# Optimization experiments

Measured on AMD Instinct MI355X. Metric: run time of the kernel, lower is better.

Reference implementation:

```python
import jax, jax.numpy as jnp
import numpy as np

B, S, L, D, C_ENC, H = 8, 4096, 77, 1280, 2048, 20
DH = D // H          # 64
SCALE = DH ** -0.5


def setup_inputs() -> dict:
    key = jax.random.key(0)
    ks = jax.random.split(key, 8)
    return {
        "hidden_states": jax.random.normal(ks[0], (B, S, D), jnp.float32),
        "encoder_hidden_states": jax.random.normal(ks[1], (B, L, C_ENC), jnp.float32),
        "region_state": jax.random.uniform(ks[2], (B, S, L), jnp.float32),
        "Wq": jax.random.normal(ks[3], (D, D), jnp.float32) * 0.02,
        "Wk": jax.random.normal(ks[4], (C_ENC, D), jnp.float32) * 0.02,
        "Wv": jax.random.normal(ks[5], (C_ENC, D), jnp.float32) * 0.02,
        "Wo": jax.random.normal(ks[6], (D, D), jnp.float32) * 0.02,
        "bo": jnp.zeros((D,), jnp.float32),
        "sigma": jnp.ones((1,), jnp.float32) * 14.6,
    }


def reference(hidden_states, encoder_hidden_states, region_state, Wq, Wk, Wv, Wo, bo, sigma):
    # QKV projections (dense GEMMs)
    q = (hidden_states @ Wq).reshape(B, S, H, DH)            # [B,S,H,dh]
    k = (encoder_hidden_states @ Wk).reshape(B, L, H, DH)    # [B,L,H,dh]
    v = (encoder_hidden_states @ Wv).reshape(B, L, H, DH)
    # scaled attention scores (baddbmm with beta=0 == plain scaled matmul)
    scores = jnp.einsum('bshd,blhd->bhsl', q, k) * SCALE      # [B,H,S,L]
    # region-prompt bias: weight_func(w, sigma, qk) = w * log(1 + 0.1*sigma) * qk.max()
    # repeat_interleave over heads == broadcast over the head axis
    bias = region_state * (jnp.log1p(sigma[0] * 0.1) * scores.max())  # [B,S,L]
    scores = scores + bias[:, None, :, :]
    probs = jax.nn.softmax(scores, axis=-1)
    out = jnp.einsum('bhsl,blhd->bshd', probs, v).reshape(B, S, D)
    # output projection (to_out[0]); to_out[1] is dropout (identity at eval)
    return out @ Wo + bo
```

## Files before the change

kernel.cpp:

```cpp
#include <hip/hip_runtime.h>
#include <hip/hip_bf16.h>
#include <math.h>

#define NB 8
#define NS 4096
#define NL 77
#define NLP 80
#define NLPV 96
#define ND 1280
#define NC 2048
#define NH 20
#define NDH 64
#define QK_SCALE 0.125f

typedef __attribute__((ext_vector_type(4))) float f32x4;
typedef __attribute__((ext_vector_type(8))) short bf16x8;

static __device__ __forceinline__ void gload_lds16(const void* g, void* l) {
  __builtin_amdgcn_global_load_lds(
      (const __attribute__((address_space(1))) void*)g,
      (__attribute__((address_space(3))) void*)l, 16, 0, 0);
}

#define BAR() do { asm volatile("" ::: "memory"); __builtin_amdgcn_s_barrier(); asm volatile("" ::: "memory"); } while (0)
#define LGKM0() asm volatile("s_waitcnt lgkmcnt(0)" ::: "memory")

__global__ void cvt_bf16_kern(const float* __restrict__ in,
                              __hip_bfloat16* __restrict__ out, long n)
{
  long i = ((long)blockIdx.x * blockDim.x + threadIdx.x) * 4;
  long stride = (long)gridDim.x * blockDim.x * 4;
  for (; i < n; i += stride) {
    float4 v = *reinterpret_cast<const float4*>(in + i);
    union { __hip_bfloat16 h[4]; ushort4 u; } r;
    r.h[0] = __float2bfloat16(v.x);
    r.h[1] = __float2bfloat16(v.y);
    r.h[2] = __float2bfloat16(v.z);
    r.h[3] = __float2bfloat16(v.w);
    *reinterpret_cast<ushort4*>(out + i) = r.u;
  }
}

__global__ void transpose_bf16_kern(const float* __restrict__ in,
                                    __hip_bfloat16* __restrict__ out,
                                    int rows, int cols)
{
  __shared__ float t[32][33];
  int c0 = blockIdx.x * 32, r0 = blockIdx.y * 32;
  int tx = threadIdx.x, ty = threadIdx.y;
  for (int i = ty; i < 32; i += 8) {
    int r = r0 + i, c = c0 + tx;
    t[i][tx] = (r < rows && c < cols) ? in[(long)r * cols + c] : 0.f;
  }
  __syncthreads();
  for (int i = ty; i < 32; i += 8) {
    int oc = c0 + i, orr = r0 + tx;
    if (oc < cols && orr < rows)
      out[(long)oc * rows + orr] = __float2bfloat16(t[tx][i]);
  }
}

__global__ __launch_bounds__(256)
void gemm_bt_kern(const __hip_bfloat16* __restrict__ A,
                  const __hip_bfloat16* __restrict__ Bt,
                  void* __restrict__ C, const float* __restrict__ bias,
                  int M, int N, int K, int mode)
{
  __shared__ __align__(16) __hip_bfloat16 As[128 * 32];
  __shared__ __align__(16) __hip_bfloat16 Bs[128 * 32];
  const int t = threadIdx.x;
  const int lane = t & 63;
  const int w = t >> 6;
  const int wm = w >> 1, wn = w & 1;
  const int lr = lane & 15, hi = lane >> 4, lk = hi * 8;
  const long m0 = (long)blockIdx.x * 128;
  const long n0 = (long)blockIdx.y * 128;

  f32x4 acc[4][4];
#pragma unroll
  for (int mi = 0; mi < 4; ++mi)
#pragma unroll
    for (int ni = 0; ni < 4; ++ni) acc[mi][ni] = {0.f, 0.f, 0.f, 0.f};

  for (int k0 = 0; k0 < K; k0 += 32) {
    __syncthreads();
#pragma unroll
    for (int rnd = 0; rnd < 2; ++rnd) {
      int idx = rnd * 256 + t;
      int row = idx >> 2, kpp = (idx & 3) * 8;
      long arow = m0 + row; if (arow >= M) arow = M - 1;
      gload_lds16(A + arow * K + k0 + kpp, (void*)(As + idx * 8));
      long brow = n0 + row;
      gload_lds16(Bt + brow * K + k0 + kpp, (void*)(Bs + idx * 8));
    }
    __syncthreads();

    bf16x8 af[4], bfr[4];
#pragma unroll
    for (int i = 0; i < 4; ++i) {
      af[i]  = *reinterpret_cast<const bf16x8*>(As + (wm * 64 + i * 16 + lr) * 32 + lk);
      bfr[i] = *reinterpret_cast<const bf16x8*>(Bs + (wn * 64 + i * 16 + lr) * 32 + lk);
    }
#pragma unroll
    for (int mi = 0; mi < 4; ++mi)
#pragma unroll
      for (int ni = 0; ni < 4; ++ni)
        acc[mi][ni] = __builtin_amdgcn_mfma_f32_16x16x32_bf16(af[mi], bfr[ni], acc[mi][ni], 0, 0, 0);
  }

#pragma unroll
  for (int mi = 0; mi < 4; ++mi) {
#pragma unroll
    for (int r = 0; r < 4; ++r) {
      long row = m0 + wm * 64 + mi * 16 + hi * 4 + r;
      if (row < M) {
#pragma unroll
        for (int ni = 0; ni < 4; ++ni) {
          long col = n0 + wn * 64 + ni * 16 + lr;
          if (mode == 0)
            ((__hip_bfloat16*)C)[row * N + col] = __float2bfloat16(acc[mi][ni][r]);
          else
            ((float*)C)[row * N + col] = acc[mi][ni][r] + bias[col];
        }
      }
    }
  }
}

__global__ __launch_bounds__(256, 2)
void gemm128_kern(const __hip_bfloat16* __restrict__ A,
                  const __hip_bfloat16* __restrict__ Bt,
                  void* __restrict__ C, const float* __restrict__ bias,
                  int M, int N, int K, int mode)
{
  __shared__ __align__(16) __hip_bfloat16 sm[32768];
  char* smc = (char*)sm;

  const int t = threadIdx.x, lane = t & 63, w = t >> 6;
  const int wm = w >> 1, wn = w & 1;
  const int lr = lane & 15, hi = lane >> 4;
  const int sw = lr & 7;

  int nwg = gridDim.x;
  int cpx = nwg >> 3;
  int swz = (blockIdx.x & 7) * cpx + (blockIdx.x >> 3);
  int nxt = N >> 7;
  int mt = swz / nxt, ntile = swz - mt * nxt;
  const long m0 = (long)mt * 128, n0 = (long)ntile * 128;

  const int srow  = t >> 3;
  const int skoff = ((t & 7) ^ (srow & 7)) * 8;
  const int sdst  = t * 16;

  f32x4 acc[4][4];
#pragma unroll
  for (int mi = 0; mi < 4; ++mi)
#pragma unroll
    for (int ni = 0; ni < 4; ++ni) acc[mi][ni] = {0.f, 0.f, 0.f, 0.f};

  auto stageA = [&](int b, int kt) {
#pragma unroll
    for (int c = 0; c < 4; ++c)
      gload_lds16(A + (m0 + c * 32 + srow) * (long)K + kt * 64 + skoff,
                  (void*)(smc + b * 16384 + c * 4096 + sdst));
  };
  auto stageB = [&](int b, int kt) {
#pragma unroll
    for (int c = 0; c < 4; ++c)
      gload_lds16(Bt + (n0 + c * 32 + srow) * (long)K + kt * 64 + skoff,
                  (void*)(smc + 32768 + b * 16384 + c * 4096 + sdst));
  };

  const int NT = K >> 6;
  stageA(0, 0); stageB(0, 0);
  stageA(1, 1); stageB(1, 1);
  asm volatile("s_waitcnt vmcnt(8)" ::: "memory");
  BAR();

  for (int t2 = 0; t2 < NT; ++t2) {
    const int b = t2 & 1;
    const char* pa = smc + b * 16384;
    const char* pb = smc + 32768 + b * 16384;
    const bool pf = (t2 + 2 < NT);

    bf16x8 af[4][2], bfr[4][2];
#pragma unroll
    for (int mi = 0; mi < 4; ++mi) {
      int row = wm * 64 + mi * 16 + lr;
#pragma unroll
      for (int kk = 0; kk < 2; ++kk)
        af[mi][kk] = *reinterpret_cast<const bf16x8*>(
            pa + row * 128 + ((((kk * 4 + hi) ^ sw)) << 4));
    }
#pragma unroll
    for (int ni = 0; ni < 4; ++ni) {
      int row = wn * 64 + ni * 16 + lr;
#pragma unroll
      for (int kk = 0; kk < 2; ++kk)
        bfr[ni][kk] = *reinterpret_cast<const bf16x8*>(
            pb + row * 128 + ((((kk * 4 + hi) ^ sw)) << 4));
    }
    __builtin_amdgcn_s_setprio(1);
#pragma unroll
    for (int mi = 0; mi < 4; ++mi)
#pragma unroll
      for (int ni = 0; ni < 4; ++ni) {
        acc[mi][ni] = __builtin_amdgcn_mfma_f32_16x16x32_bf16(af[mi][0], bfr[ni][0], acc[mi][ni], 0, 0, 0);
        acc[mi][ni] = __builtin_amdgcn_mfma_f32_16x16x32_bf16(af[mi][1], bfr[ni][1], acc[mi][ni], 0, 0, 0);
      }
    __builtin_amdgcn_s_setprio(0);

    LGKM0();
    BAR();
    if (pf) { stageA(b, t2 + 2); stageB(b, t2 + 2); }
    if (pf) { asm volatile("s_waitcnt vmcnt(8)" ::: "memory"); }
    else    { asm volatile("s_waitcnt vmcnt(0)" ::: "memory"); }
    BAR();
  }

  if (mode == 0) {
#pragma unroll
    for (int mi = 0; mi < 4; ++mi)
#pragma unroll
      for (int r = 0; r < 4; ++r) {
        long row = m0 + wm * 64 + mi * 16 + hi * 4 + r;
#pragma unroll
        for (int ni = 0; ni < 4; ++ni) {
          long col = n0 + wn * 64 + ni * 16 + lr;
          ((__hip_bfloat16*)C)[row * N + col] = __float2bfloat16(acc[mi][ni][r]);
        }
      }
  } else {
    float bv[4];
#pragma unroll
    for (int ni = 0; ni < 4; ++ni) bv[ni] = bias[n0 + wn * 64 + ni * 16 + lr];
#pragma unroll
    for (int mi = 0; mi < 4; ++mi)
#pragma unroll
      for (int r = 0; r < 4; ++r) {
        long row = m0 + wm * 64 + mi * 16 + hi * 4 + r;
#pragma unroll
        for (int ni = 0; ni < 4; ++ni) {
          long col = n0 + wn * 64 + ni * 16 + lr;
          ((float*)C)[row * N + col] = acc[mi][ni][r] + bv[ni];
        }
      }
  }
}

__global__ void repack_kv_kern(const __hip_bfloat16* __restrict__ kvc,
                               __hip_bfloat16* __restrict__ kp,
                               __hip_bfloat16* __restrict__ vt)
{
  int idx = blockIdx.x * 256 + threadIdx.x;
  const __hip_bfloat16 z = __float2bfloat16(0.f);
  if (idx < NB * NLP * ND) {
    int d = idx % ND;
    int l = (idx / ND) % NLP;
    int b = idx / (ND * NLP);
    kp[idx] = (l < NL) ? kvc[((long)(b * NL + l)) * 2560 + d] : z;
  }
  if (idx < NB * NH * NDH * NLPV) {
    int l  = idx % NLPV;
    int dh = (idx / NLPV) % NDH;
    int h  = (idx / (NLPV * NDH)) % NH;
    int b  = idx / (NLPV * NDH * NH);
    vt[idx] = (l < NL) ? kvc[((long)(b * NL + l)) * 2560 + ND + h * NDH + dh] : z;
  }
}

__global__ __launch_bounds__(256)
void qk_max_kern(const __hip_bfloat16* __restrict__ qb,
                 const __hip_bfloat16* __restrict__ kp,
                 float* __restrict__ bmax)
{
  int t = threadIdx.x, lane = t & 63, wi = t >> 6;
  int b = blockIdx.z, h = blockIdx.y;
  int lr = lane & 15, lk = (lane >> 4) * 8;

  bf16x8 bk[5][2];
#pragma unroll
  for (int lt = 0; lt < 5; ++lt) {
    const __hip_bfloat16* Kr = kp + ((long)(b * NLP + lt * 16 + lr)) * ND + h * NDH + lk;
    bk[lt][0] = *reinterpret_cast<const bf16x8*>(Kr);
    bk[lt][1] = *reinterpret_cast<const bf16x8*>(Kr + 32);
  }

  float m = -1e30f;
#pragma unroll
  for (int st = 0; st < 4; ++st) {
    int s0 = blockIdx.x * 256 + wi * 64 + st * 16;
    const __hip_bfloat16* Qp = qb + ((long)(b * NS + s0 + lr)) * ND + h * NDH + lk;
    bf16x8 aq0 = *reinterpret_cast<const bf16x8*>(Qp);
    bf16x8 aq1 = *reinterpret_cast<const bf16x8*>(Qp + 32);
#pragma unroll
    for (int lt = 0; lt < 5; ++lt) {
      f32x4 sc = {0.f, 0.f, 0.f, 0.f};
      sc = __builtin_amdgcn_mfma_f32_16x16x32_bf16(aq0, bk[lt][0], sc, 0, 0, 0);
      sc = __builtin_amdgcn_mfma_f32_16x16x32_bf16(aq1, bk[lt][1], sc, 0, 0, 0);
      bool valid = (lt < 4) || (lr < 13);
      if (valid) {
#pragma unroll
        for (int r = 0; r < 4; ++r) m = fmaxf(m, sc[r]);
      }
    }
  }
#pragma unroll
  for (int k = 32; k >= 1; k >>= 1) m = fmaxf(m, __shfl_xor(m, k));

  __shared__ float wmx[4];
  if (lane == 0) wmx[wi] = m;
  __syncthreads();
  if (t == 0) {
    float mm = fmaxf(fmaxf(wmx[0], wmx[1]), fmaxf(wmx[2], wmx[3]));
    long bid = ((long)blockIdx.z * gridDim.y + blockIdx.y) * gridDim.x + blockIdx.x;
    bmax[bid] = mm * QK_SCALE;
  }
}

__global__ void reduce_max_kern(const float* __restrict__ bm, int n,
                                const float* __restrict__ sigma,
                                float* __restrict__ cb)
{
  __shared__ float sm[256];
  float m = -1e30f;
  for (int i = threadIdx.x; i < n; i += 256) m = fmaxf(m, bm[i]);
  sm[threadIdx.x] = m;
  __syncthreads();
  for (int s = 128; s > 0; s >>= 1) {
    if (threadIdx.x < (unsigned)s) sm[threadIdx.x] = fmaxf(sm[threadIdx.x], sm[threadIdx.x + s]);
    __syncthreads();
  }
  if (threadIdx.x == 0) cb[0] = log1pf(sigma[0] * 0.1f) * sm[0];
}

__global__ __launch_bounds__(256)
void attn_kern(const __hip_bfloat16* __restrict__ qb,
               const __hip_bfloat16* __restrict__ kp,
               const __hip_bfloat16* __restrict__ vt,
               const float* __restrict__ rs,
               const float* __restrict__ cb,
               __hip_bfloat16* __restrict__ ao_out)
{
  __shared__ __align__(16) __hip_bfloat16 pl[4][16][NLPV];
  int t = threadIdx.x, lane = t & 63, wi = t >> 6;
  int b = blockIdx.z, h = blockIdx.y;
  int lr = lane & 15, hi = lane >> 4, lk = hi * 8;
  const float c = cb[0];

  bf16x8 bk[5][2];
#pragma unroll
  for (int lt = 0; lt < 5; ++lt) {
    const __hip_bfloat16* Kr = kp + ((long)(b * NLP + lt * 16 + lr)) * ND + h * NDH + lk;
    bk[lt][0] = *reinterpret_cast<const bf16x8*>(Kr);
    bk[lt][1] = *reinterpret_cast<const bf16x8*>(Kr + 32);
  }
#pragma unroll
  for (int r = 0; r < 4; ++r)
    pl[wi][hi * 4 + r][80 + lr] = __float2bfloat16(0.f);

  const __hip_bfloat16* Vb = vt + ((long)((b * NH + h) * NDH)) * NLPV;

#pragma unroll
  for (int st = 0; st < 4; ++st) {
    int s0 = blockIdx.x * 256 + wi * 64 + st * 16;
    const __hip_bfloat16* Qp = qb + ((long)(b * NS + s0 + lr)) * ND + h * NDH + lk;
    bf16x8 aq0 = *reinterpret_cast<const bf16x8*>(Qp);
    bf16x8 aq1 = *reinterpret_cast<const bf16x8*>(Qp + 32);

    f32x4 sc[5];
#pragma unroll
    for (int lt = 0; lt < 5; ++lt) {
      f32x4 z = {0.f, 0.f, 0.f, 0.f};
      z = __builtin_amdgcn_mfma_f32_16x16x32_bf16(aq0, bk[lt][0], z, 0, 0, 0);
      sc[lt] = __builtin_amdgcn_mfma_f32_16x16x32_bf16(aq1, bk[lt][1], z, 0, 0, 0);
    }

    float sv[5][4];
    float pm[4] = {-1e30f, -1e30f, -1e30f, -1e30f};
#pragma unroll
    for (int lt = 0; lt < 5; ++lt) {
      int l = lt * 16 + lr;
#pragma unroll
      for (int r = 0; r < 4; ++r) {
        if (l < NL) {
          int srow = s0 + hi * 4 + r;
          float v = sc[lt][r] * QK_SCALE + rs[((long)(b * NS + srow)) * NL + l] * c;
          sv[lt][r] = v;
          pm[r] = fmaxf(pm[r], v);
        } else {
          sv[lt][r] = -1e30f;
        }
      }
    }
#pragma unroll
    for (int r = 0; r < 4; ++r)
#pragma unroll
      for (int k = 8; k >= 1; k >>= 1) pm[r] = fmaxf(pm[r], __shfl_xor(pm[r], k));

    float p[5][4];
    float psum[4] = {0.f, 0.f, 0.f, 0.f};
#pragma unroll
    for (int lt = 0; lt < 5; ++lt) {
      int l = lt * 16 + lr;
#pragma unroll
      for (int r = 0; r < 4; ++r) {
        float e = (l < NL) ? __expf(sv[lt][r] - pm[r]) : 0.f;
        p[lt][r] = e;
        psum[r] += e;
      }
    }
#pragma unroll
    for (int r = 0; r < 4; ++r)
#pragma unroll
      for (int k = 8; k >= 1; k >>= 1) psum[r] += __shfl_xor(psum[r], k);
    float rinv[4];
#pragma unroll
    for (int r = 0; r < 4; ++r) rinv[r] = 1.f / psum[r];

    LGKM0();

#pragma unroll
    for (int lt = 0; lt < 5; ++lt)
#pragma unroll
      for (int r = 0; r < 4; ++r)
        pl[wi][hi * 4 + r][lt * 16 + lr] = __float2bfloat16(p[lt][r]);

    LGKM0();

    f32x4 ao[4];
#pragma unroll
    for (int nt = 0; nt < 4; ++nt) ao[nt] = {0.f, 0.f, 0.f, 0.f};
#pragma unroll
    for (int ks = 0; ks < 3; ++ks) {
      bf16x8 pa = *reinterpret_cast<const bf16x8*>(&pl[wi][lr][ks * 32 + lk]);
#pragma unroll
      for (int nt = 0; nt < 4; ++nt) {
        bf16x8 bv = *reinterpret_cast<const bf16x8*>(Vb + ((long)(nt * 16 + lr)) * NLPV + ks * 32 + lk);
        ao[nt] = __builtin_amdgcn_mfma_f32_16x16x32_bf16(pa, bv, ao[nt], 0, 0, 0);
      }
    }

#pragma unroll
    for (int nt = 0; nt < 4; ++nt)
#pragma unroll
      for (int r = 0; r < 4; ++r) {
        int srow = s0 + hi * 4 + r;
        ao_out[((long)(b * NS + srow)) * ND + h * NDH + nt * 16 + lr] =
            __float2bfloat16(ao[nt][r] * rinv[r]);
      }
  }
}

extern "C" void kernel_launch(void* const* d_in, const int* in_sizes, int n_in,
                              void* d_out, int out_size, void* d_ws, size_t ws_size,
                              hipStream_t stream)
{
  const float* hs    = (const float*)d_in[0];
  const float* ehs   = (const float*)d_in[1];
  const float* rs    = (const float*)d_in[2];
  const float* Wq    = (const float*)d_in[3];
  const float* Wk    = (const float*)d_in[4];
  const float* Wv    = (const float*)d_in[5];
  const float* Wo    = (const float*)d_in[6];
  const float* bo    = (const float*)d_in[7];
  const float* sigma = (const float*)d_in[8];
  float* out = (float*)d_out;

  char* ws = (char*)d_ws;
  size_t off = 0;
  auto alloc = [&](size_t bytes) {
    void* p = ws + off;
    off = (off + bytes + 255) & ~(size_t)255;
    return p;
  };
  __hip_bfloat16* hsb  = (__hip_bfloat16*)alloc((size_t)NB * NS * ND * 2);
  __hip_bfloat16* qb   = (__hip_bfloat16*)alloc((size_t)NB * NS * ND * 2);
  __hip_bfloat16* wqt  = (__hip_bfloat16*)alloc((size_t)ND * ND * 2);
  __hip_bfloat16* wkvt = (__hip_bfloat16*)alloc((size_t)2560 * NC * 2);
  __hip_bfloat16* wot  = (__hip_bfloat16*)alloc((size_t)ND * ND * 2);
  __hip_bfloat16* ehsb = (__hip_bfloat16*)alloc((size_t)NB * NL * NC * 2);
  __hip_bfloat16* kvc  = (__hip_bfloat16*)alloc((size_t)NB * NL * 2560 * 2);
  __hip_bfloat16* kp   = (__hip_bfloat16*)alloc((size_t)NB * NLP * ND * 2);
  __hip_bfloat16* vt   = (__hip_bfloat16*)alloc((size_t)NB * NH * NDH * NLPV * 2);
  float* bmax = (float*)alloc(10240 * 4);
  float* cb   = (float*)alloc(256);

  cvt_bf16_kern<<<2048, 256, 0, stream>>>(hs, hsb, (long)NB * NS * ND);
  cvt_bf16_kern<<<512, 256, 0, stream>>>(ehs, ehsb, (long)NB * NL * NC);

  transpose_bf16_kern<<<dim3(40, 40), dim3(32, 8), 0, stream>>>(Wq, wqt, ND, ND);
  transpose_bf16_kern<<<dim3(40, 64), dim3(32, 8), 0, stream>>>(Wk, wkvt, NC, ND);
  transpose_bf16_kern<<<dim3(40, 64), dim3(32, 8), 0, stream>>>(Wv, wkvt + (size_t)ND * NC, NC, ND);
  transpose_bf16_kern<<<dim3(40, 40), dim3(32, 8), 0, stream>>>(Wo, wot, ND, ND);

  gemm128_kern<<<2560, 256, 0, stream>>>(hsb, wqt, qb, nullptr, NB * NS, ND, ND, 0);

  gemm_bt_kern<<<dim3(5, 20), 256, 0, stream>>>(ehsb, wkvt, kvc, nullptr, NB * NL, 2560, NC, 0);

  repack_kv_kern<<<3840, 256, 0, stream>>>(kvc, kp, vt);

  qk_max_kern<<<dim3(16, NH, NB), 256, 0, stream>>>(qb, kp, bmax);
  reduce_max_kern<<<1, 256, 0, stream>>>(bmax, 16 * NH * NB, sigma, cb);

  attn_kern<<<dim3(16, NH, NB), 256, 0, stream>>>(qb, kp, vt, rs, cb, hsb);

  gemm128_kern<<<2560, 256, 0, stream>>>(hsb, wot, out, bo, NB * NS, ND, ND, 1);
}
```

Measured before the change: 502.5 us.

## Fuse fp32-to-bf16 conversion into Q GEMM and use single-buffered GEMM

Removes the standalone conversion kernel for hidden_states. The Q projection GEMM now loads fp32 tiles straight into LDS and converts them to bf16 while building MFMA fragments. The GEMM is also restructured: the double-buffered async prefetch pipeline is replaced by a single-buffered load, sync, compute loop, and launch bounds are raised to 4 blocks per CU so occupancy can hide latency. This saves a full read and write pass over the 8x4096x1280 activation, but A-tile traffic doubles in the GEMM and load/compute overlap inside a block is lost.

```diff
diff --git a/kernel.cpp b/kernel.cpp
--- a/kernel.cpp
+++ b/kernel.cpp
@@ -22,7 +22,6 @@
       (__attribute__((address_space(3))) void*)l, 16, 0, 0);
 }
 
-#define BAR() do { asm volatile("" ::: "memory"); __builtin_amdgcn_s_barrier(); asm volatile("" ::: "memory"); } while (0)
 #define LGKM0() asm volatile("s_waitcnt lgkmcnt(0)" ::: "memory")
 
 __global__ void cvt_bf16_kern(const float* __restrict__ in,
@@ -127,19 +126,19 @@
   }
 }
 
-__global__ __launch_bounds__(256, 2)
-void gemm128_kern(const __hip_bfloat16* __restrict__ A,
+template<bool AF32>
+__global__ __launch_bounds__(256, 4)
+void gemm_sb_kern(const void* __restrict__ Av,
                   const __hip_bfloat16* __restrict__ Bt,
                   void* __restrict__ C, const float* __restrict__ bias,
                   int M, int N, int K, int mode)
 {
-  __shared__ __align__(16) __hip_bfloat16 sm[32768];
-  char* smc = (char*)sm;
+  constexpr int ABYTES = AF32 ? 32768 : 16384;
+  __shared__ __align__(16) char smc[ABYTES + 16384];
 
   const int t = threadIdx.x, lane = t & 63, w = t >> 6;
   const int wm = w >> 1, wn = w & 1;
   const int lr = lane & 15, hi = lane >> 4;
-  const int sw = lr & 7;
 
   int nwg = gridDim.x;
   int cpx = nwg >> 3;
@@ -148,49 +147,70 @@
   int mt = swz / nxt, ntile = swz - mt * nxt;
   const long m0 = (long)mt * 128, n0 = (long)ntile * 128;
 
-  const int srow  = t >> 3;
-  const int skoff = ((t & 7) ^ (srow & 7)) * 8;
-  const int sdst  = t * 16;
-
   f32x4 acc[4][4];
 #pragma unroll
   for (int mi = 0; mi < 4; ++mi)
 #pragma unroll
     for (int ni = 0; ni < 4; ++ni) acc[mi][ni] = {0.f, 0.f, 0.f, 0.f};
 
-  auto stageA = [&](int b, int kt) {
-#pragma unroll
-    for (int c = 0; c < 4; ++c)
-      gload_lds16(A + (m0 + c * 32 + srow) * (long)K + kt * 64 + skoff,
-                  (void*)(smc + b * 16384 + c * 4096 + sdst));
-  };
-  auto stageB = [&](int b, int kt) {
-#pragma unroll
-    for (int c = 0; c < 4; ++c)
-      gload_lds16(Bt + (n0 + c * 32 + srow) * (long)K + kt * 64 + skoff,
-                  (void*)(smc + 32768 + b * 16384 + c * 4096 + sdst));
-  };
-
   const int NT = K >> 6;
-  stageA(0, 0); stageB(0, 0);
-  stageA(1, 1); stageB(1, 1);
-  asm volatile("s_waitcnt vmcnt(8)" ::: "memory");
-  BAR();
-
-  for (int t2 = 0; t2 < NT; ++t2) {
-    const int b = t2 & 1;
-    const char* pa = smc + b * 16384;
-    const char* pb = smc + 32768 + b * 16384;
-    const bool pf = (t2 + 2 < NT);
+  for (int kt = 0; kt < NT; ++kt) {
+    __syncthreads();
+    if constexpr (AF32) {
+      const float* A = (const float*)Av;
+      int row0 = t >> 4, slot = t & 15;
+      int eoff = (slot ^ row0) * 4;
+#pragma unroll
+      for (int c = 0; c < 8; ++c) {
+        int row = c * 16 + row0;
+        gload_lds16(A + (m0 + row) * (long)K + kt * 64 + eoff,
+                    (void*)(smc + c * 4096 + t * 16));
+      }
+    } else {
+      const __hip_bfloat16* A = (const __hip_bfloat16*)Av;
+      int row0 = t >> 3, slot = t & 7;
+      int eoff = (slot ^ (row0 & 7)) * 8;
+#pragma unroll
+      for (int c = 0; c < 4; ++c) {
+        int row = c * 32 + row0;
+        gload_lds16(A + (m0 + row) * (long)K + kt * 64 + eoff,
+                    (void*)(smc + c * 4096 + t * 16));
+      }
+    }
+    {
+      int row0 = t >> 3, slot = t & 7;
+      int eoff = (slot ^ (row0 & 7)) * 8;
+#pragma unroll
+      for (int c = 0; c < 4; ++c) {
+        int row = c * 32 + row0;
+        gload_lds16(Bt + (n0 + row) * (long)K + kt * 64 + eoff,
+                    (void*)(smc + ABYTES + c * 4096 + t * 16));
+      }
+    }
+    __syncthreads();
 
     bf16x8 af[4][2], bfr[4][2];
 #pragma unroll
     for (int mi = 0; mi < 4; ++mi) {
       int row = wm * 64 + mi * 16 + lr;
 #pragma unroll
-      for (int kk = 0; kk < 2; ++kk)
-        af[mi][kk] = *reinterpret_cast<const bf16x8*>(
-            pa + row * 128 + ((((kk * 4 + hi) ^ sw)) << 4));
+      for (int kk = 0; kk < 2; ++kk) {
+        if constexpr (AF32) {
+          int s0 = 8 * kk + 2 * hi;
+          f32x4 v0 = *reinterpret_cast<const f32x4*>(smc + row * 256 + (((s0)     ^ lr) << 4));
+          f32x4 v1 = *reinterpret_cast<const f32x4*>(smc + row * 256 + (((s0 + 1) ^ lr) << 4));
+          bf16x8 r;
+#pragma unroll
+          for (int e = 0; e < 4; ++e) {
+            r[e]     = (short)__bfloat16_as_ushort(__float2bfloat16(v0[e]));
+            r[e + 4] = (short)__bfloat16_as_ushort(__float2bfloat16(v1[e]));
+          }
+          af[mi][kk] = r;
+        } else {
+          af[mi][kk] = *reinterpret_cast<const bf16x8*>(
+              smc + row * 128 + (((kk * 4 + hi) ^ (lr & 7)) << 4));
+        }
+      }
     }
 #pragma unroll
     for (int ni = 0; ni < 4; ++ni) {
@@ -198,9 +218,8 @@
 #pragma unroll
       for (int kk = 0; kk < 2; ++kk)
         bfr[ni][kk] = *reinterpret_cast<const bf16x8*>(
-            pb + row * 128 + ((((kk * 4 + hi) ^ sw)) << 4));
-    }
-    __builtin_amdgcn_s_setprio(1);
+            smc + ABYTES + row * 128 + (((kk * 4 + hi) ^ (lr & 7)) << 4));
+    }
 #pragma unroll
     for (int mi = 0; mi < 4; ++mi)
 #pragma unroll
@@ -208,14 +227,6 @@
         acc[mi][ni] = __builtin_amdgcn_mfma_f32_16x16x32_bf16(af[mi][0], bfr[ni][0], acc[mi][ni], 0, 0, 0);
         acc[mi][ni] = __builtin_amdgcn_mfma_f32_16x16x32_bf16(af[mi][1], bfr[ni][1], acc[mi][ni], 0, 0, 0);
       }
-    __builtin_amdgcn_s_setprio(0);
-
-    LGKM0();
-    BAR();
-    if (pf) { stageA(b, t2 + 2); stageB(b, t2 + 2); }
-    if (pf) { asm volatile("s_waitcnt vmcnt(8)" ::: "memory"); }
-    else    { asm volatile("s_waitcnt vmcnt(0)" ::: "memory"); }
-    BAR();
   }
 
   if (mode == 0) {
@@ -474,7 +485,7 @@
     off = (off + bytes + 255) & ~(size_t)255;
     return p;
   };
-  __hip_bfloat16* hsb  = (__hip_bfloat16*)alloc((size_t)NB * NS * ND * 2);
+  __hip_bfloat16* aob  = (__hip_bfloat16*)alloc((size_t)NB * NS * ND * 2);
   __hip_bfloat16* qb   = (__hip_bfloat16*)alloc((size_t)NB * NS * ND * 2);
   __hip_bfloat16* wqt  = (__hip_bfloat16*)alloc((size_t)ND * ND * 2);
   __hip_bfloat16* wkvt = (__hip_bfloat16*)alloc((size_t)2560 * NC * 2);
@@ -486,7 +497,6 @@
   float* bmax = (float*)alloc(10240 * 4);
   float* cb   = (float*)alloc(256);
 
-  cvt_bf16_kern<<<2048, 256, 0, stream>>>(hs, hsb, (long)NB * NS * ND);
   cvt_bf16_kern<<<512, 256, 0, stream>>>(ehs, ehsb, (long)NB * NL * NC);
 
   transpose_bf16_kern<<<dim3(40, 40), dim3(32, 8), 0, stream>>>(Wq, wqt, ND, ND);
@@ -494,7 +504,7 @@
   transpose_bf16_kern<<<dim3(40, 64), dim3(32, 8), 0, stream>>>(Wv, wkvt + (size_t)ND * NC, NC, ND);
   transpose_bf16_kern<<<dim3(40, 40), dim3(32, 8), 0, stream>>>(Wo, wot, ND, ND);
 
-  gemm128_kern<<<2560, 256, 0, stream>>>(hsb, wqt, qb, nullptr, NB * NS, ND, ND, 0);
+  gemm_sb_kern<true><<<2560, 256, 0, stream>>>(hs, wqt, qb, nullptr, NB * NS, ND, ND, 0);
 
   gemm_bt_kern<<<dim3(5, 20), 256, 0, stream>>>(ehsb, wkvt, kvc, nullptr, NB * NL, 2560, NC, 0);
 
@@ -503,7 +513,7 @@
   qk_max_kern<<<dim3(16, NH, NB), 256, 0, stream>>>(qb, kp, bmax);
   reduce_max_kern<<<1, 256, 0, stream>>>(bmax, 16 * NH * NB, sigma, cb);
 
-  attn_kern<<<dim3(16, NH, NB), 256, 0, stream>>>(qb, kp, vt, rs, cb, hsb);
-
-  gemm128_kern<<<2560, 256, 0, stream>>>(hsb, wot, out, bo, NB * NS, ND, ND, 1);
-}
+  attn_kern<<<dim3(16, NH, NB), 256, 0, stream>>>(qb, kp, vt, rs, cb, aob);
+
+  gemm_sb_kern<false><<<2560, 256, 0, stream>>>(aob, wot, out, bo, NB * NS, ND, ND, 1);
+}
```

New measurement: 529.0 us. +5.3%, slower.

## Fuse QK max reduction into Q projection GEMM epilogue and reorder barrier

Applied to the files above, without the earlier changes.

The Q projection GEMM now runs after the K/V repack and, in a templated mode, writes its bf16 output tile into LDS and computes the per-tile max of QK^T scores against K directly in its epilogue. This removes the separate qk_max kernel, which re-read all of Q from global memory. The main loop also moves the LDS wait, barrier and next-tile prefetch to before the MFMA block, so global loads overlap with the math. The costs are a longer epilogue, extra K loads per block, and more registers in the GEMM.

```diff
diff --git a/kernel.cpp b/kernel.cpp
--- a/kernel.cpp
+++ b/kernel.cpp
@@ -127,11 +127,14 @@
   }
 }
 
+template<int MODE>
 __global__ __launch_bounds__(256, 2)
 void gemm128_kern(const __hip_bfloat16* __restrict__ A,
                   const __hip_bfloat16* __restrict__ Bt,
                   void* __restrict__ C, const float* __restrict__ bias,
-                  int M, int N, int K, int mode)
+                  const __hip_bfloat16* __restrict__ kp,
+                  float* __restrict__ bmax,
+                  int M, int N, int K)
 {
   __shared__ __align__(16) __hip_bfloat16 sm[32768];
   char* smc = (char*)sm;
@@ -200,6 +203,10 @@
         bfr[ni][kk] = *reinterpret_cast<const bf16x8*>(
             pb + row * 128 + ((((kk * 4 + hi) ^ sw)) << 4));
     }
+    LGKM0();
+    BAR();
+    if (pf) { stageA(b, t2 + 2); stageB(b, t2 + 2); }
+
     __builtin_amdgcn_s_setprio(1);
 #pragma unroll
     for (int mi = 0; mi < 4; ++mi)
@@ -210,27 +217,12 @@
       }
     __builtin_amdgcn_s_setprio(0);
 
-    LGKM0();
-    BAR();
-    if (pf) { stageA(b, t2 + 2); stageB(b, t2 + 2); }
     if (pf) { asm volatile("s_waitcnt vmcnt(8)" ::: "memory"); }
     else    { asm volatile("s_waitcnt vmcnt(0)" ::: "memory"); }
     BAR();
   }
 
-  if (mode == 0) {
-#pragma unroll
-    for (int mi = 0; mi < 4; ++mi)
-#pragma unroll
-      for (int r = 0; r < 4; ++r) {
-        long row = m0 + wm * 64 + mi * 16 + hi * 4 + r;
-#pragma unroll
-        for (int ni = 0; ni < 4; ++ni) {
-          long col = n0 + wn * 64 + ni * 16 + lr;
-          ((__hip_bfloat16*)C)[row * N + col] = __float2bfloat16(acc[mi][ni][r]);
-        }
-      }
-  } else {
+  if constexpr (MODE == 1) {
     float bv[4];
 #pragma unroll
     for (int ni = 0; ni < 4; ++ni) bv[ni] = bias[n0 + wn * 64 + ni * 16 + lr];
@@ -245,6 +237,70 @@
           ((float*)C)[row * N + col] = acc[mi][ni][r] + bv[ni];
         }
       }
+  } else {
+    __hip_bfloat16* qsl = (__hip_bfloat16*)smc;
+#pragma unroll
+    for (int mi = 0; mi < 4; ++mi)
+#pragma unroll
+      for (int r = 0; r < 4; ++r) {
+        int rowl = wm * 64 + mi * 16 + hi * 4 + r;
+        long row = m0 + rowl;
+#pragma unroll
+        for (int ni = 0; ni < 4; ++ni) {
+          int col = wn * 64 + ni * 16 + lr;
+          __hip_bfloat16 v = __float2bfloat16(acc[mi][ni][r]);
+          ((__hip_bfloat16*)C)[row * N + n0 + col] = v;
+          if constexpr (MODE == 2) {
+            int bw = (col >> 3) ^ (rowl & 7);
+            qsl[rowl * 128 + (bw << 3) + (col & 7)] = v;
+          }
+        }
+      }
+    if constexpr (MODE == 2) {
+      LGKM0();
+      BAR();
+      const int bb = (int)(m0 >> 12);
+      float mx = -1e30f;
+#pragma unroll
+      for (int hh = 0; hh < 2; ++hh) {
+        const int h = (int)(n0 >> 6) + hh;
+        bf16x8 bk0[5], bk1[5];
+#pragma unroll
+        for (int lt = 0; lt < 5; ++lt) {
+          const __hip_bfloat16* Kr = kp + ((long)(bb * NLP + lt * 16 + lr)) * ND + h * NDH + hi * 8;
+          bk0[lt] = *reinterpret_cast<const bf16x8*>(Kr);
+          bk1[lt] = *reinterpret_cast<const bf16x8*>(Kr + 32);
+        }
+#pragma unroll
+        for (int su = 0; su < 2; ++su) {
+          int qrow = (w * 2 + su) * 16 + lr;
+          int bi0 = (hh * 8 + hi)     ^ sw;
+          int bi1 = (hh * 8 + 4 + hi) ^ sw;
+          bf16x8 aq0 = *reinterpret_cast<const bf16x8*>(qsl + qrow * 128 + (bi0 << 3));
+          bf16x8 aq1 = *reinterpret_cast<const bf16x8*>(qsl + qrow * 128 + (bi1 << 3));
+#pragma unroll
+          for (int lt = 0; lt < 5; ++lt) {
+            f32x4 sc = {0.f, 0.f, 0.f, 0.f};
+            sc = __builtin_amdgcn_mfma_f32_16x16x32_bf16(aq0, bk0[lt], sc, 0, 0, 0);
+            sc = __builtin_amdgcn_mfma_f32_16x16x32_bf16(aq1, bk1[lt], sc, 0, 0, 0);
+            if ((lt < 4) || (lr < 13)) {
+#pragma unroll
+              for (int r = 0; r < 4; ++r) mx = fmaxf(mx, sc[r]);
+            }
+          }
+        }
+      }
+#pragma unroll
+      for (int k = 32; k >= 1; k >>= 1) mx = fmaxf(mx, __shfl_xor(mx, k));
+      float* wmx = (float*)(smc + 32768);
+      if (lane == 0) wmx[w] = mx;
+      LGKM0();
+      BAR();
+      if (t == 0) {
+        float mm = fmaxf(fmaxf(wmx[0], wmx[1]), fmaxf(wmx[2], wmx[3]));
+        bmax[blockIdx.x] = mm * QK_SCALE;
+      }
+    }
   }
 }
 
@@ -266,55 +322,6 @@
     int h  = (idx / (NLPV * NDH)) % NH;
     int b  = idx / (NLPV * NDH * NH);
     vt[idx] = (l < NL) ? kvc[((long)(b * NL + l)) * 2560 + ND + h * NDH + dh] : z;
-  }
-}
-
-__global__ __launch_bounds__(256)
-void qk_max_kern(const __hip_bfloat16* __restrict__ qb,
-                 const __hip_bfloat16* __restrict__ kp,
-                 float* __restrict__ bmax)
-{
-  int t = threadIdx.x, lane = t & 63, wi = t >> 6;
-  int b = blockIdx.z, h = blockIdx.y;
-  int lr = lane & 15, lk = (lane >> 4) * 8;
-
-  bf16x8 bk[5][2];
-#pragma unroll
-  for (int lt = 0; lt < 5; ++lt) {
-    const __hip_bfloat16* Kr = kp + ((long)(b * NLP + lt * 16 + lr)) * ND + h * NDH + lk;
-    bk[lt][0] = *reinterpret_cast<const bf16x8*>(Kr);
-    bk[lt][1] = *reinterpret_cast<const bf16x8*>(Kr + 32);
-  }
-
-  float m = -1e30f;
-#pragma unroll
-  for (int st = 0; st < 4; ++st) {
-    int s0 = blockIdx.x * 256 + wi * 64 + st * 16;
-    const __hip_bfloat16* Qp = qb + ((long)(b * NS + s0 + lr)) * ND + h * NDH + lk;
-    bf16x8 aq0 = *reinterpret_cast<const bf16x8*>(Qp);
-    bf16x8 aq1 = *reinterpret_cast<const bf16x8*>(Qp + 32);
-#pragma unroll
-    for (int lt = 0; lt < 5; ++lt) {
-      f32x4 sc = {0.f, 0.f, 0.f, 0.f};
-      sc = __builtin_amdgcn_mfma_f32_16x16x32_bf16(aq0, bk[lt][0], sc, 0, 0, 0);
-      sc = __builtin_amdgcn_mfma_f32_16x16x32_bf16(aq1, bk[lt][1], sc, 0, 0, 0);
-      bool valid = (lt < 4) || (lr < 13);
-      if (valid) {
-#pragma unroll
-        for (int r = 0; r < 4; ++r) m = fmaxf(m, sc[r]);
-      }
-    }
-  }
-#pragma unroll
-  for (int k = 32; k >= 1; k >>= 1) m = fmaxf(m, __shfl_xor(m, k));
-
-  __shared__ float wmx[4];
-  if (lane == 0) wmx[wi] = m;
-  __syncthreads();
-  if (t == 0) {
-    float mm = fmaxf(fmaxf(wmx[0], wmx[1]), fmaxf(wmx[2], wmx[3]));
-    long bid = ((long)blockIdx.z * gridDim.y + blockIdx.y) * gridDim.x + blockIdx.x;
-    bmax[bid] = mm * QK_SCALE;
   }
 }
 
@@ -494,16 +501,14 @@
   transpose_bf16_kern<<<dim3(40, 64), dim3(32, 8), 0, stream>>>(Wv, wkvt + (size_t)ND * NC, NC, ND);
   transpose_bf16_kern<<<dim3(40, 40), dim3(32, 8), 0, stream>>>(Wo, wot, ND, ND);
 
-  gemm128_kern<<<2560, 256, 0, stream>>>(hsb, wqt, qb, nullptr, NB * NS, ND, ND, 0);
-
   gemm_bt_kern<<<dim3(5, 20), 256, 0, stream>>>(ehsb, wkvt, kvc, nullptr, NB * NL, 2560, NC, 0);
-
   repack_kv_kern<<<3840, 256, 0, stream>>>(kvc, kp, vt);
 
-  qk_max_kern<<<dim3(16, NH, NB), 256, 0, stream>>>(qb, kp, bmax);
-  reduce_max_kern<<<1, 256, 0, stream>>>(bmax, 16 * NH * NB, sigma, cb);
+  gemm128_kern<2><<<2560, 256, 0, stream>>>(hsb, wqt, qb, nullptr, kp, bmax, NB * NS, ND, ND);
+
+  reduce_max_kern<<<1, 256, 0, stream>>>(bmax, 2560, sigma, cb);
 
   attn_kern<<<dim3(16, NH, NB), 256, 0, stream>>>(qb, kp, vt, rs, cb, hsb);
 
-  gemm128_kern<<<2560, 256, 0, stream>>>(hsb, wot, out, bo, NB * NS, ND, ND, 1);
-}
+  gemm128_kern<1><<<2560, 256, 0, stream>>>(hsb, wot, out, bo, nullptr, nullptr, NB * NS, ND, ND);
+}
```

After: 482.3 us. 4.0% less time.
